# Performance work log

Measured on AMD Instinct MI355X. Metric: run time of the kernel, lower is better.

Reference implementation:

```python
import jax, jax.numpy as jnp
import numpy as np
from jax import lax

C = 128
HEADS = 8
HID = 256  # int(C * 2.0)
B, H, W = 8, 128, 128
EPS_LN = 1e-5
EPS_NORM = 1e-12


def _dwconv(x, w, pad):
    # x: [B,C,H,W], w: [C,1,kh,kw] depthwise
    return lax.conv_general_dilated(
        x, w, window_strides=(1, 1), padding=[(pad, pad), (pad, pad)],
        dimension_numbers=("NCHW", "OIHW", "NCHW"), feature_group_count=x.shape[1])


def _conv1x1(x, w):
    # w: [O, I] pointwise conv
    return jnp.einsum("oi,bihw->bohw", w, x)


def _layernorm_c(x, gamma, beta):
    # torch: reshape to [B, HW, C], LayerNorm over C, reshape back == LN over channel axis
    mu = jnp.mean(x, axis=1, keepdims=True)
    var = jnp.mean(jnp.square(x - mu), axis=1, keepdims=True)
    xn = (x - mu) * lax.rsqrt(var + EPS_LN)
    return xn * gamma[None, :, None, None] + beta[None, :, None, None]


def _l2norm(x):
    n = jnp.sqrt(jnp.sum(jnp.square(x), axis=-1, keepdims=True))
    return x / jnp.maximum(n, EPS_NORM)


def _mdta(x, qkv_w, qkv_dw, temperature, attn_proj):
    b, c, h, w = x.shape
    qkv = _dwconv(_conv1x1(x, qkv_w), qkv_dw, pad=1)  # [B,3C,H,W]
    q, k, v = jnp.split(qkv, 3, axis=1)
    hd = c // HEADS
    q = q.reshape(b, HEADS, hd, h * w)
    k = k.reshape(b, HEADS, hd, h * w)
    v = v.reshape(b, HEADS, hd, h * w)
    q, k = _l2norm(q), _l2norm(k)
    attn = jax.nn.softmax(jnp.einsum("bhdn,bhen->bhde", q, k) * temperature, axis=-1)
    out = jnp.einsum("bhde,bhen->bhdn", attn, v).reshape(b, c, h, w)
    return _conv1x1(out, attn_proj)


def _gdfn2(x, pin_w, c1_w, c3_w, c5_w, pout_w):
    x = _conv1x1(x, pin_w)  # [B,HID,H,W]
    x1 = x * c1_w[None, :, 0, 0, 0, None, None]  # depthwise 1x1 == per-channel scale
    x3 = _dwconv(x, c3_w, pad=1)
    x5 = _dwconv(x, c5_w, pad=2)
    g = jax.nn.gelu(x1, approximate=False)
    gated = jnp.concatenate([g * x3, g * x5], axis=1)  # [B,2*HID,H,W]
    return _conv1x1(gated, pout_w)


def setup_inputs() -> dict:
    key = jax.random.key(0)
    ks = jax.random.split(key, 12)
    s = 0.05
    return {
        "x": jax.random.normal(ks[0], (B, C, H, W), jnp.float32),
        "ln1_w": jnp.ones((C,), jnp.float32),
        "ln1_b": jnp.zeros((C,), jnp.float32),
        "qkv_w": jax.random.normal(ks[1], (3 * C, C), jnp.float32) * s,
        "qkv_dw": jax.random.normal(ks[2], (3 * C, 1, 3, 3), jnp.float32) * s,
        "temperature": jnp.ones((1, HEADS, 1, 1), jnp.float32),
        "attn_proj": jax.random.normal(ks[3], (C, C), jnp.float32) * s,
        "ln2_w": jnp.ones((C,), jnp.float32),
        "ln2_b": jnp.zeros((C,), jnp.float32),
        "pin_w": jax.random.normal(ks[4], (HID, C), jnp.float32) * s,
        "c1_w": jax.random.normal(ks[5], (HID, 1, 1, 1), jnp.float32) * s,
        "c3_w": jax.random.normal(ks[6], (HID, 1, 3, 3), jnp.float32) * s,
        "c5_w": jax.random.normal(ks[7], (HID, 1, 5, 5), jnp.float32) * s,
        "pout_w": jax.random.normal(ks[8], (C, 2 * HID), jnp.float32) * s,
    }


def reference(x, ln1_w, ln1_b, qkv_w, qkv_dw, temperature, attn_proj,
              ln2_w, ln2_b, pin_w, c1_w, c3_w, c5_w, pout_w):
    x = x + _mdta(_layernorm_c(x, ln1_w, ln1_b), qkv_w, qkv_dw, temperature, attn_proj)
    x = x + _gdfn2(_layernorm_c(x, ln2_w, ln2_b), pin_w, c1_w, c3_w, c5_w, pout_w)
    return x
```

## Files before the change

kernel.cpp:

```cpp
#include <hip/hip_runtime.h>
#include <type_traits>

typedef unsigned short ushort;
typedef unsigned int uint;
typedef __bf16 bf16x8 __attribute__((ext_vector_type(8)));
typedef unsigned short ushort8v __attribute__((ext_vector_type(8)));
typedef float f32x4 __attribute__((ext_vector_type(4)));

__device__ __forceinline__ float b2f(ushort u) {
    unsigned int x = ((unsigned int)u) << 16;
    float f;
    __builtin_memcpy(&f, &x, 4);
    return f;
}
__device__ __forceinline__ ushort f2bf(float f) {
    unsigned int x;
    __builtin_memcpy(&x, &f, 4);
    unsigned int r = x + 0x7fffu + ((x >> 16) & 1u);
    return (ushort)(r >> 16);
}
__device__ __forceinline__ float u2f_lo(uint u) {
    uint x = u << 16;
    float f;
    __builtin_memcpy(&f, &x, 4);
    return f;
}
__device__ __forceinline__ float u2f_hi(uint u) {
    uint x = u & 0xffff0000u;
    float f;
    __builtin_memcpy(&f, &x, 4);
    return f;
}
__device__ __forceinline__ uint packbf(float a, float b) {
    return (uint)f2bf(a) | ((uint)f2bf(b) << 16);
}

#define NPIX 16384
#define PSTRIDE 136

__device__ __forceinline__ size_t tadr(int b, int CH, int tile, int ch, int off) {
    return (((size_t)b * 256 + tile) * CH + ch) * 64 + off;
}

__device__ __forceinline__ void stage_plane(ushort* pl, const ushort* __restrict__ src,
                                            int b, int c, int CH, int tid) {
    uint* plu = (uint*)pl;
    for (int i = tid; i < 784; i += 256) {
        int idx;
        if (i < 136) idx = i;
        else if (i < 272) idx = 8840 + (i - 136);
        else {
            int j = i - 272;
            int r = (j >> 2) + 2;
            int cs = j & 3;
            idx = r * 68 + (cs == 0 ? 0 : 64 + cs);
        }
        plu[idx] = 0u;
    }
    for (int i = tid; i < 2048; i += 256) {
        int row = i >> 4, xg = (i & 15) << 3;
        int px0 = row * 128 + xg;
        uint4 v = *(const uint4*)&src[tadr(b, CH, px0 >> 6, c, px0 & 63)];
        uint* dst = (uint*)&pl[(row + 2) * PSTRIDE + xg + 2];
        dst[0] = v.x; dst[1] = v.y; dst[2] = v.z; dst[3] = v.w;
    }
    __syncthreads();
}

__device__ __forceinline__ void unpack12(const ushort* rowp, float* cc) {
    const uint* rp = (const uint*)rowp;
    uint4 u = *(const uint4*)rp;
    uint2 v = *(const uint2*)(rp + 4);
    cc[0] = u2f_lo(u.x); cc[1] = u2f_hi(u.x);
    cc[2] = u2f_lo(u.y); cc[3] = u2f_hi(u.y);
    cc[4] = u2f_lo(u.z); cc[5] = u2f_hi(u.z);
    cc[6] = u2f_lo(u.w); cc[7] = u2f_hi(u.w);
    cc[8] = u2f_lo(v.x); cc[9] = u2f_hi(v.x);
    cc[10] = u2f_lo(v.y); cc[11] = u2f_hi(v.y);
}

__global__ __launch_bounds__(256) void wcvt(const float* __restrict__ s0, ushort* __restrict__ d0, int n0,
                                            const float* __restrict__ s1, ushort* __restrict__ d1, int n1,
                                            const float* __restrict__ s2, ushort* __restrict__ d2, int n2) {
    int i = blockIdx.x * 256 + threadIdx.x;
    if (i < n0) d0[i] = f2bf(s0[i]);
    else if (i < n0 + n1) d1[i - n0] = f2bf(s1[i - n0]);
    else if (i < n0 + n1 + n2) d2[i - n0 - n1] = f2bf(s2[i - n0 - n1]);
}

template <int O, typename TIN>
__global__ __launch_bounds__(256) void ln_gemm_mfma(const TIN* __restrict__ xin,
                                                    const ushort* __restrict__ Wb,
                                                    const float* __restrict__ gamma,
                                                    const float* __restrict__ beta,
                                                    ushort* __restrict__ out) {
    __shared__ ushort xs[64][136];
    __shared__ float red[2][4][64];
    __shared__ float mu[64], rs[64];
    __shared__ float gl[128], bl[128];

    const int blk = blockIdx.x;
    const int b = blk >> 8;
    const int tile = blk & 255;
    const int tid = threadIdx.x;

    if constexpr (std::is_same<TIN, float>::value) {
        const float* xb = xin + (size_t)b * 128 * NPIX + tile * 64;
        for (int i = tid; i < 1024; i += 256) {
            int p = i & 63, cg = i >> 6;
            const float* src = xb + (size_t)(cg * 8) * NPIX + p;
            ushort8v u;
#pragma unroll
            for (int j = 0; j < 8; j++) u[j] = f2bf(src[(size_t)j * NPIX]);
            *(ushort8v*)&xs[p][cg * 8] = u;
        }
    } else {
        const ushort* xb = xin + tadr(b, 128, tile, 0, 0);
        for (int i = tid; i < 1024; i += 256) {
            int p = i & 63, cg = i >> 6;
            ushort8v u;
#pragma unroll
            for (int j = 0; j < 8; j++) u[j] = xb[(cg * 8 + j) * 64 + p];
            *(ushort8v*)&xs[p][cg * 8] = u;
        }
    }
    if (tid < 128) {
        gl[tid] = gamma[tid];
        bl[tid] = beta[tid];
    }
    __syncthreads();

    {
        const int p = tid & 63, part = tid >> 6;
        float s = 0.f, ss = 0.f;
#pragma unroll
        for (int q = 0; q < 4; q++) {
            ushort8v u = *(const ushort8v*)&xs[p][part * 32 + q * 8];
#pragma unroll
            for (int j = 0; j < 8; j++) {
                float v = b2f(u[j]);
                s += v;
                ss += v * v;
            }
        }
        red[0][part][p] = s;
        red[1][part][p] = ss;
    }
    __syncthreads();
    if (tid < 64) {
        float s = red[0][0][tid] + red[0][1][tid] + red[0][2][tid] + red[0][3][tid];
        float ss = red[1][0][tid] + red[1][1][tid] + red[1][2][tid] + red[1][3][tid];
        float m = s * (1.f / 128.f);
        float var = ss * (1.f / 128.f) - m * m;
        mu[tid] = m;
        rs[tid] = rsqrtf(var + 1e-5f);
    }
    __syncthreads();
    {
        const int p = tid & 63, part = tid >> 6;
        const float mp = mu[p], rp = rs[p];
#pragma unroll
        for (int q = 0; q < 4; q++) {
            int c0 = part * 32 + q * 8;
            ushort8v u = *(const ushort8v*)&xs[p][c0];
            ushort8v o;
#pragma unroll
            for (int j = 0; j < 8; j++) {
                float v = b2f(u[j]);
                o[j] = f2bf((v - mp) * rp * gl[c0 + j] + bl[c0 + j]);
            }
            *(ushort8v*)&xs[p][c0] = o;
        }
    }
    __syncthreads();

    const int wv = tid >> 6, lane = tid & 63;
    const int lr = lane & 15, lg = lane >> 4;

    bf16x8 bfr[4][4];
#pragma unroll
    for (int t = 0; t < 4; t++)
#pragma unroll
        for (int kc = 0; kc < 4; kc++)
            bfr[t][kc] = __builtin_bit_cast(bf16x8, *(const ushort8v*)&xs[t * 16 + lr][kc * 32 + lg * 8]);

    constexpr int MT = O / 64;
#pragma unroll 1
    for (int mt = 0; mt < MT; mt++) {
        const int o0 = (wv * MT + mt) * 16;
        bf16x8 afr[4];
#pragma unroll
        for (int kc = 0; kc < 4; kc++)
            afr[kc] = __builtin_bit_cast(bf16x8,
                *(const ushort8v*)&Wb[(size_t)(o0 + lr) * 128 + kc * 32 + lg * 8]);
        f32x4 acc[4] = {{0.f, 0.f, 0.f, 0.f}, {0.f, 0.f, 0.f, 0.f}, {0.f, 0.f, 0.f, 0.f}, {0.f, 0.f, 0.f, 0.f}};
#pragma unroll
        for (int kc = 0; kc < 4; kc++)
#pragma unroll
            for (int t = 0; t < 4; t++)
                acc[t] = __builtin_amdgcn_mfma_f32_16x16x32_bf16(afr[kc], bfr[t][kc], acc[t], 0, 0, 0);
#pragma unroll
        for (int t = 0; t < 4; t++)
#pragma unroll
            for (int r = 0; r < 4; r++) {
                int o = o0 + lg * 4 + r;
                out[tadr(b, O, tile, o, t * 16 + lr)] = f2bf(acc[t][r]);
            }
    }
}

__global__ __launch_bounds__(256) void dwconv3_lds(const ushort* __restrict__ in,
                                                   const float* __restrict__ wdw,
                                                   ushort* __restrict__ out, int CH) {
    __shared__ ushort pl[132 * PSTRIDE];
    const int c = blockIdx.x;
    const int b = blockIdx.y;
    const int tid = threadIdx.x;

    float w[9];
#pragma unroll
    for (int j = 0; j < 9; j++) w[j] = wdw[c * 9 + j];

    stage_plane(pl, in, b, c, CH, tid);

    const int x = (tid & 15) * 8;
    const int ybase = tid >> 4;
#pragma unroll 1
    for (int k = 0; k < 8; k++) {
        const int y = k * 16 + ybase;
        float a[8];
#pragma unroll
        for (int p = 0; p < 8; p++) a[p] = 0.f;
#pragma unroll
        for (int ky = 0; ky < 3; ky++) {
            float cc[12];
            unpack12(&pl[(y + ky + 1) * PSTRIDE + x], cc);
#pragma unroll
            for (int kx = 0; kx < 3; kx++) {
                float wv = w[ky * 3 + kx];
#pragma unroll
                for (int p = 0; p < 8; p++) a[p] += cc[p + kx + 1] * wv;
            }
        }
        const int px0 = (y << 7) + x;
        uint4 o;
        o.x = packbf(a[0], a[1]);
        o.y = packbf(a[2], a[3]);
        o.z = packbf(a[4], a[5]);
        o.w = packbf(a[6], a[7]);
        *(uint4*)&out[tadr(b, CH, px0 >> 6, c, px0 & 63)] = o;
    }
}

__global__ __launch_bounds__(256) void dw_gated(const ushort* __restrict__ t,
                                                const float* __restrict__ w3_,
                                                const float* __restrict__ w5_,
                                                const float* __restrict__ c1w,
                                                ushort* __restrict__ gated) {
    __shared__ ushort pl[132 * PSTRIDE];
    const int c = blockIdx.x;
    const int b = blockIdx.y;
    const int tid = threadIdx.x;

    float w3[9], w5[25];
#pragma unroll
    for (int j = 0; j < 9; j++) w3[j] = w3_[c * 9 + j];
#pragma unroll
    for (int j = 0; j < 25; j++) w5[j] = w5_[c * 25 + j];
    const float c1v = c1w[c];

    stage_plane(pl, t, b, c, 256, tid);

    const int x = (tid & 15) * 8;
    const int ybase = tid >> 4;
#pragma unroll 1
    for (int k = 0; k < 8; k++) {
        const int y = k * 16 + ybase;
        float a5[8], a3[8], tc[8];
#pragma unroll
        for (int p = 0; p < 8; p++) { a5[p] = 0.f; a3[p] = 0.f; }
#pragma unroll
        for (int ky = 0; ky < 5; ky++) {
            float cc[12];
            unpack12(&pl[(y + ky) * PSTRIDE + x], cc);
#pragma unroll
            for (int kx = 0; kx < 5; kx++) {
                float wv = w5[ky * 5 + kx];
#pragma unroll
                for (int p = 0; p < 8; p++) a5[p] += cc[p + kx] * wv;
            }
            if (ky >= 1 && ky <= 3) {
#pragma unroll
                for (int kx = 0; kx < 3; kx++) {
                    float wv = w3[(ky - 1) * 3 + kx];
#pragma unroll
                    for (int p = 0; p < 8; p++) a3[p] += cc[p + kx + 1] * wv;
                }
            }
            if (ky == 2) {
#pragma unroll
                for (int p = 0; p < 8; p++) tc[p] = cc[p + 2];
            }
        }
        const int px0 = (y << 7) + x;
        uint4 o3, o5;
        float g[8];
#pragma unroll
        for (int p = 0; p < 8; p++) {
            float x1 = tc[p] * c1v;
            g[p] = x1 * __builtin_amdgcn_rcpf(1.f + __expf(-1.702f * x1));
        }
        o3.x = packbf(g[0] * a3[0], g[1] * a3[1]);
        o3.y = packbf(g[2] * a3[2], g[3] * a3[3]);
        o3.z = packbf(g[4] * a3[4], g[5] * a3[5]);
        o3.w = packbf(g[6] * a3[6], g[7] * a3[7]);
        o5.x = packbf(g[0] * a5[0], g[1] * a5[1]);
        o5.y = packbf(g[2] * a5[2], g[3] * a5[3]);
        o5.z = packbf(g[4] * a5[4], g[5] * a5[5]);
        o5.w = packbf(g[6] * a5[6], g[7] * a5[7]);
        *(uint4*)&gated[tadr(b, 512, px0 >> 6, c, px0 & 63)] = o3;
        *(uint4*)&gated[tadr(b, 512, px0 >> 6, 256 + c, px0 & 63)] = o5;
    }
}

__global__ __launch_bounds__(256) void attn_M(const ushort* __restrict__ qkv,
                                              const float* __restrict__ temp,
                                              const float* __restrict__ attn_proj,
                                              ushort* __restrict__ M) {
    __shared__ float Sp[4][16][16];
    __shared__ float QSS[4][16], KSS[4][16];
    __shared__ float A[16][17];

    const int bh = blockIdx.x, b = bh >> 3, h = bh & 7;
    const int tid = threadIdx.x;
    const int w = tid >> 6, lane = tid & 63;
    const int lr = lane & 15, lg = lane >> 4;

    const size_t qbase = (((size_t)b * 256 + w * 64) * 384 + h * 16 + lr) * 64 + lg * 8;
    const size_t kbase = qbase + (size_t)128 * 64;

    f32x4 acc = {0.f, 0.f, 0.f, 0.f};
    f32x4 accq = {0.f, 0.f, 0.f, 0.f};
    f32x4 acck = {0.f, 0.f, 0.f, 0.f};
#pragma unroll 2
    for (int it = 0; it < 128; it++) {
        size_t off = (size_t)(it >> 1) * (384 * 64) + (it & 1) * 32;
        bf16x8 qf = __builtin_bit_cast(bf16x8, *(const ushort8v*)(qkv + qbase + off));
        bf16x8 kf = __builtin_bit_cast(bf16x8, *(const ushort8v*)(qkv + kbase + off));
        acc = __builtin_amdgcn_mfma_f32_16x16x32_bf16(qf, kf, acc, 0, 0, 0);
        accq = __builtin_amdgcn_mfma_f32_16x16x32_bf16(qf, qf, accq, 0, 0, 0);
        acck = __builtin_amdgcn_mfma_f32_16x16x32_bf16(kf, kf, acck, 0, 0, 0);
    }
#pragma unroll
    for (int r = 0; r < 4; r++) Sp[w][lg * 4 + r][lr] = acc[r];
    if (lg == (lr >> 2)) {
        QSS[w][lr] = accq[lr & 3];
        KSS[w][lr] = acck[lr & 3];
    }
    __syncthreads();

    const int d = tid >> 4, e = tid & 15;
    float S = Sp[0][d][e] + Sp[1][d][e] + Sp[2][d][e] + Sp[3][d][e];
    float nq = fmaxf(sqrtf(QSS[0][d] + QSS[1][d] + QSS[2][d] + QSS[3][d]), 1e-12f);
    float nk = fmaxf(sqrtf(KSS[0][e] + KSS[1][e] + KSS[2][e] + KSS[3][e]), 1e-12f);
    float logit = S / (nq * nk) * temp[h];
    float m = logit;
    for (int off = 8; off; off >>= 1) m = fmaxf(m, __shfl_xor(m, off, 64));
    float ex = expf(logit - m);
    float sum = ex;
    for (int off = 8; off; off >>= 1) sum += __shfl_xor(sum, off, 64);
    A[d][e] = ex / sum;
    __syncthreads();

    for (int i = tid; i < 2048; i += 256) {
        int o = i >> 4, ee = i & 15;
        float acc2 = 0.f;
#pragma unroll
        for (int dd = 0; dd < 16; dd++) acc2 += attn_proj[o * 128 + h * 16 + dd] * A[dd][ee];
        M[((size_t)b * 128 + o) * 128 + h * 16 + ee] = f2bf(acc2);
    }
}

__global__ __launch_bounds__(256) void mv_res_mfma(const ushort* __restrict__ qkv,
                                                   const ushort* __restrict__ Mb16,
                                                   const float* __restrict__ x,
                                                   ushort* __restrict__ x2) {
    __shared__ ushort vs[64][136];
    const int blk = blockIdx.x;
    const int b = blk >> 8;
    const int tile = blk & 255;
    const int tid = threadIdx.x;

    const ushort* vb = qkv + tadr(b, 384, tile, 256, 0);
    for (int i = tid; i < 1024; i += 256) {
        int p = i & 63, cg = i >> 6;
        ushort8v u;
#pragma unroll
        for (int j = 0; j < 8; j++) u[j] = vb[(cg * 8 + j) * 64 + p];
        *(ushort8v*)&vs[p][cg * 8] = u;
    }
    __syncthreads();

    const int wv = tid >> 6, lane = tid & 63;
    const int lr = lane & 15, lg = lane >> 4;

    bf16x8 bfr[4][4];
#pragma unroll
    for (int t = 0; t < 4; t++)
#pragma unroll
        for (int kc = 0; kc < 4; kc++)
            bfr[t][kc] = __builtin_bit_cast(bf16x8, *(const ushort8v*)&vs[t * 16 + lr][kc * 32 + lg * 8]);

    const ushort* Mb = Mb16 + (size_t)b * 128 * 128;
#pragma unroll 1
    for (int mt = 0; mt < 2; mt++) {
        const int o0 = (wv * 2 + mt) * 16;
        bf16x8 afr[4];
#pragma unroll
        for (int kc = 0; kc < 4; kc++)
            afr[kc] = __builtin_bit_cast(bf16x8,
                *(const ushort8v*)&Mb[(size_t)(o0 + lr) * 128 + kc * 32 + lg * 8]);
        f32x4 acc[4] = {{0.f, 0.f, 0.f, 0.f}, {0.f, 0.f, 0.f, 0.f}, {0.f, 0.f, 0.f, 0.f}, {0.f, 0.f, 0.f, 0.f}};
#pragma unroll
        for (int kc = 0; kc < 4; kc++)
#pragma unroll
            for (int t = 0; t < 4; t++)
                acc[t] = __builtin_amdgcn_mfma_f32_16x16x32_bf16(afr[kc], bfr[t][kc], acc[t], 0, 0, 0);
#pragma unroll
        for (int t = 0; t < 4; t++)
#pragma unroll
            for (int r = 0; r < 4; r++) {
                int o = o0 + lg * 4 + r;
                float xv = x[((size_t)b * 128 + o) * NPIX + tile * 64 + t * 16 + lr];
                x2[tadr(b, 128, tile, o, t * 16 + lr)] = f2bf(xv + acc[t][r]);
            }
    }
}

__global__ __launch_bounds__(256) void gdfn_mfma(const ushort* __restrict__ gated,
                                                 const ushort* __restrict__ x2,
                                                 const ushort* __restrict__ pout_b,
                                                 float* __restrict__ out) {
    __shared__ ushort gs[64][72];

    const int blk = blockIdx.x;
    const int b = blk >> 8;
    const int tile = blk & 255;
    const int tid = threadIdx.x;
    const int wv = tid >> 6, lane = tid & 63;
    const int lr = lane & 15, lg = lane >> 4;

    const ushort* gb = gated + tadr(b, 512, tile, 0, 0);

    f32x4 acc[2][4];
#pragma unroll
    for (int mt = 0; mt < 2; mt++)
#pragma unroll
        for (int tt = 0; tt < 4; tt++) acc[mt][tt] = (f32x4){0.f, 0.f, 0.f, 0.f};

#pragma unroll 1
    for (int kb = 0; kb < 8; kb++) {
        __syncthreads();
        for (int i = tid; i < 512; i += 256) {
            int p = i & 63, kg = i >> 6;
            const ushort* src = gb + (kb * 64 + kg * 8) * 64 + p;
            ushort8v u;
#pragma unroll
            for (int j = 0; j < 8; j++) u[j] = src[j * 64];
            *(ushort8v*)&gs[p][kg * 8] = u;
        }
        __syncthreads();

        bf16x8 bfrg[4][2];
#pragma unroll
        for (int tt = 0; tt < 4; tt++)
#pragma unroll
            for (int kc = 0; kc < 2; kc++)
                bfrg[tt][kc] = __builtin_bit_cast(bf16x8, *(const ushort8v*)&gs[tt * 16 + lr][kc * 32 + lg * 8]);

#pragma unroll
        for (int mt = 0; mt < 2; mt++) {
            const int o0 = (wv * 2 + mt) * 16;
            bf16x8 afr[2];
#pragma unroll
            for (int kc = 0; kc < 2; kc++)
                afr[kc] = __builtin_bit_cast(bf16x8,
                    *(const ushort8v*)&pout_b[(size_t)(o0 + lr) * 512 + kb * 64 + kc * 32 + lg * 8]);
#pragma unroll
            for (int kc = 0; kc < 2; kc++)
#pragma unroll
                for (int tt = 0; tt < 4; tt++)
                    acc[mt][tt] = __builtin_amdgcn_mfma_f32_16x16x32_bf16(afr[kc], bfrg[tt][kc], acc[mt][tt], 0, 0, 0);
        }
    }

#pragma unroll
    for (int mt = 0; mt < 2; mt++)
#pragma unroll
        for (int tt = 0; tt < 4; tt++)
#pragma unroll
            for (int r = 0; r < 4; r++) {
                int o = (wv * 2 + mt) * 16 + lg * 4 + r;
                float xv = b2f(x2[tadr(b, 128, tile, o, tt * 16 + lr)]);
                out[((size_t)b * 128 + o) * NPIX + tile * 64 + tt * 16 + lr] = xv + acc[mt][tt][r];
            }
}

extern "C" void kernel_launch(void* const* d_in, const int* in_sizes, int n_in,
                              void* d_out, int out_size, void* d_ws, size_t ws_size,
                              hipStream_t stream) {
    const float* x = (const float*)d_in[0];
    const float* ln1_w = (const float*)d_in[1];
    const float* ln1_b = (const float*)d_in[2];
    const float* qkv_w = (const float*)d_in[3];
    const float* qkv_dw = (const float*)d_in[4];
    const float* temperature = (const float*)d_in[5];
    const float* attn_proj = (const float*)d_in[6];
    const float* ln2_w = (const float*)d_in[7];
    const float* ln2_b = (const float*)d_in[8];
    const float* pin_w = (const float*)d_in[9];
    const float* c1_w = (const float*)d_in[10];
    const float* c3_w = (const float*)d_in[11];
    const float* c5_w = (const float*)d_in[12];
    const float* pout_w = (const float*)d_in[13];
    float* out = (float*)d_out;

    char* ws = (char*)d_ws;
    ushort* qkv_pre = (ushort*)(ws + 0);
    ushort* qkv     = (ushort*)(ws + 100663296);
    ushort* x2      = (ushort*)(ws + 201326592);
    ushort* t       = (ushort*)(ws + 0);
    ushort* gated   = (ushort*)(ws + 67108864);
    ushort* Mb16    = (ushort*)(ws + 235151360);
    ushort* qkv_wb  = (ushort*)(ws + 235413504);
    ushort* pin_wb  = (ushort*)(ws + 235511808);
    ushort* pout_wb = (ushort*)(ws + 235577344);

    wcvt<<<576, 256, 0, stream>>>(qkv_w, qkv_wb, 49152, pin_w, pin_wb, 32768, pout_w, pout_wb, 65536);
    ln_gemm_mfma<384, float><<<2048, 256, 0, stream>>>(x, qkv_wb, ln1_w, ln1_b, qkv_pre);
    dwconv3_lds<<<dim3(384, 8), 256, 0, stream>>>(qkv_pre, qkv_dw, qkv, 384);
    attn_M<<<64, 256, 0, stream>>>(qkv, temperature, attn_proj, Mb16);
    mv_res_mfma<<<2048, 256, 0, stream>>>(qkv, Mb16, x, x2);
    ln_gemm_mfma<256, ushort><<<2048, 256, 0, stream>>>(x2, pin_wb, ln2_w, ln2_b, t);
    dw_gated<<<dim3(256, 8), 256, 0, stream>>>(t, c3_w, c5_w, c1_w, gated);
    gdfn_mfma<<<2048, 256, 0, stream>>>(gated, x2, pout_wb, out);
}
```

Measured before the change: 324.8 us.

## Fuse attention output, residual, LayerNorm2 and pin GEMM; double-buffer gdfn staging

Merges the M·V residual kernel with the second LayerNorm and pin-projection GEMM so x2 stays in LDS instead of being written and reloaded. x2 is stored pixel-major for vectorized access in the final residual. The gated-input staging in gdfn_mfma is double-buffered with register prefetch to overlap loads with MFMA work, and V/gated loads switch to vector global reads with scattered LDS writes. This removes one launch and an x2 round trip, at the cost of more LDS per block and possible LDS bank conflicts from transposed writes.

After: 320.3 us. About the same (-1.4%).

```diff
diff --git a/kernel.cpp b/kernel.cpp
--- a/kernel.cpp
+++ b/kernel.cpp
@@ -40,6 +40,9 @@
 
 __device__ __forceinline__ size_t tadr(int b, int CH, int tile, int ch, int off) {
     return (((size_t)b * 256 + tile) * CH + ch) * 64 + off;
+}
+__device__ __forceinline__ size_t padr(int b, int tile, int p, int c) {
+    return (((size_t)b * 256 + tile) * 64 + p) * 128 + c;
 }
 
 __device__ __forceinline__ void stage_plane(ushort* pl, const ushort* __restrict__ src,
@@ -88,8 +91,8 @@
     else if (i < n0 + n1 + n2) d2[i - n0 - n1] = f2bf(s2[i - n0 - n1]);
 }
 
-template <int O, typename TIN>
-__global__ __launch_bounds__(256) void ln_gemm_mfma(const TIN* __restrict__ xin,
+template <int O>
+__global__ __launch_bounds__(256) void ln_gemm_mfma(const float* __restrict__ xin,
                                                     const ushort* __restrict__ Wb,
                                                     const float* __restrict__ gamma,
                                                     const float* __restrict__ beta,
@@ -104,25 +107,14 @@
     const int tile = blk & 255;
     const int tid = threadIdx.x;
 
-    if constexpr (std::is_same<TIN, float>::value) {
-        const float* xb = xin + (size_t)b * 128 * NPIX + tile * 64;
-        for (int i = tid; i < 1024; i += 256) {
-            int p = i & 63, cg = i >> 6;
-            const float* src = xb + (size_t)(cg * 8) * NPIX + p;
-            ushort8v u;
-#pragma unroll
-            for (int j = 0; j < 8; j++) u[j] = f2bf(src[(size_t)j * NPIX]);
-            *(ushort8v*)&xs[p][cg * 8] = u;
-        }
-    } else {
-        const ushort* xb = xin + tadr(b, 128, tile, 0, 0);
-        for (int i = tid; i < 1024; i += 256) {
-            int p = i & 63, cg = i >> 6;
-            ushort8v u;
-#pragma unroll
-            for (int j = 0; j < 8; j++) u[j] = xb[(cg * 8 + j) * 64 + p];
-            *(ushort8v*)&xs[p][cg * 8] = u;
-        }
+    const float* xb = xin + (size_t)b * 128 * NPIX + tile * 64;
+    for (int i = tid; i < 1024; i += 256) {
+        int p = i & 63, cg = i >> 6;
+        const float* src = xb + (size_t)(cg * 8) * NPIX + p;
+        ushort8v u;
+#pragma unroll
+        for (int j = 0; j < 8; j++) u[j] = f2bf(src[(size_t)j * NPIX]);
+        *(ushort8v*)&xs[p][cg * 8] = u;
     }
     if (tid < 128) {
         gl[tid] = gamma[tid];
@@ -381,67 +373,19 @@
     }
 }
 
-__global__ __launch_bounds__(256) void mv_res_mfma(const ushort* __restrict__ qkv,
-                                                   const ushort* __restrict__ Mb16,
-                                                   const float* __restrict__ x,
-                                                   ushort* __restrict__ x2) {
+__global__ __launch_bounds__(256) void mv_ln_mfma(const ushort* __restrict__ qkv,
+                                                  const ushort* __restrict__ Mb16,
+                                                  const float* __restrict__ x,
+                                                  const ushort* __restrict__ pin_b,
+                                                  const float* __restrict__ gamma,
+                                                  const float* __restrict__ beta,
+                                                  ushort* __restrict__ x2,
+                                                  ushort* __restrict__ t_out) {
     __shared__ ushort vs[64][136];
-    const int blk = blockIdx.x;
-    const int b = blk >> 8;
-    const int tile = blk & 255;
-    const int tid = threadIdx.x;
-
-    const ushort* vb = qkv + tadr(b, 384, tile, 256, 0);
-    for (int i = tid; i < 1024; i += 256) {
-        int p = i & 63, cg = i >> 6;
-        ushort8v u;
-#pragma unroll
-        for (int j = 0; j < 8; j++) u[j] = vb[(cg * 8 + j) * 64 + p];
-        *(ushort8v*)&vs[p][cg * 8] = u;
-    }
-    __syncthreads();
-
-    const int wv = tid >> 6, lane = tid & 63;
-    const int lr = lane & 15, lg = lane >> 4;
-
-    bf16x8 bfr[4][4];
-#pragma unroll
-    for (int t = 0; t < 4; t++)
-#pragma unroll
-        for (int kc = 0; kc < 4; kc++)
-            bfr[t][kc] = __builtin_bit_cast(bf16x8, *(const ushort8v*)&vs[t * 16 + lr][kc * 32 + lg * 8]);
-
-    const ushort* Mb = Mb16 + (size_t)b * 128 * 128;
-#pragma unroll 1
-    for (int mt = 0; mt < 2; mt++) {
-        const int o0 = (wv * 2 + mt) * 16;
-        bf16x8 afr[4];
-#pragma unroll
-        for (int kc = 0; kc < 4; kc++)
-            afr[kc] = __builtin_bit_cast(bf16x8,
-                *(const ushort8v*)&Mb[(size_t)(o0 + lr) * 128 + kc * 32 + lg * 8]);
-        f32x4 acc[4] = {{0.f, 0.f, 0.f, 0.f}, {0.f, 0.f, 0.f, 0.f}, {0.f, 0.f, 0.f, 0.f}, {0.f, 0.f, 0.f, 0.f}};
-#pragma unroll
-        for (int kc = 0; kc < 4; kc++)
-#pragma unroll
-            for (int t = 0; t < 4; t++)
-                acc[t] = __builtin_amdgcn_mfma_f32_16x16x32_bf16(afr[kc], bfr[t][kc], acc[t], 0, 0, 0);
-#pragma unroll
-        for (int t = 0; t < 4; t++)
-#pragma unroll
-            for (int r = 0; r < 4; r++) {
-                int o = o0 + lg * 4 + r;
-                float xv = x[((size_t)b * 128 + o) * NPIX + tile * 64 + t * 16 + lr];
-                x2[tadr(b, 128, tile, o, t * 16 + lr)] = f2bf(xv + acc[t][r]);
-            }
-    }
-}
-
-__global__ __launch_bounds__(256) void gdfn_mfma(const ushort* __restrict__ gated,
-                                                 const ushort* __restrict__ x2,
-                                                 const ushort* __restrict__ pout_b,
-                                                 float* __restrict__ out) {
-    __shared__ ushort gs[64][72];
+    __shared__ ushort xs[64][136];
+    __shared__ float red[2][4][64];
+    __shared__ float mu[64], rs[64];
+    __shared__ float gl[128], bl[128];
 
     const int blk = blockIdx.x;
     const int b = blk >> 8;
@@ -450,33 +394,184 @@
     const int wv = tid >> 6, lane = tid & 63;
     const int lr = lane & 15, lg = lane >> 4;
 
+    const ushort* vb = qkv + tadr(b, 384, tile, 256, 0);
+#pragma unroll
+    for (int k = 0; k < 4; k++) {
+        int idx = tid + k * 256;
+        int c = idx & 127, pg = idx >> 7;
+        ushort8v u = *(const ushort8v*)&vb[c * 64 + pg * 8];
+#pragma unroll
+        for (int j = 0; j < 8; j++) vs[pg * 8 + j][c] = u[j];
+    }
+    if (tid < 128) {
+        gl[tid] = gamma[tid];
+        bl[tid] = beta[tid];
+    }
+    __syncthreads();
+
+    bf16x8 bfr[4][4];
+#pragma unroll
+    for (int t = 0; t < 4; t++)
+#pragma unroll
+        for (int kc = 0; kc < 4; kc++)
+            bfr[t][kc] = __builtin_bit_cast(bf16x8, *(const ushort8v*)&vs[t * 16 + lr][kc * 32 + lg * 8]);
+
+    const ushort* Mb = Mb16 + (size_t)b * 128 * 128;
+#pragma unroll 1
+    for (int mt = 0; mt < 2; mt++) {
+        const int o0 = (wv * 2 + mt) * 16;
+        bf16x8 afr[4];
+#pragma unroll
+        for (int kc = 0; kc < 4; kc++)
+            afr[kc] = __builtin_bit_cast(bf16x8,
+                *(const ushort8v*)&Mb[(size_t)(o0 + lr) * 128 + kc * 32 + lg * 8]);
+        f32x4 acc[4] = {{0.f, 0.f, 0.f, 0.f}, {0.f, 0.f, 0.f, 0.f}, {0.f, 0.f, 0.f, 0.f}, {0.f, 0.f, 0.f, 0.f}};
+#pragma unroll
+        for (int kc = 0; kc < 4; kc++)
+#pragma unroll
+            for (int t = 0; t < 4; t++)
+                acc[t] = __builtin_amdgcn_mfma_f32_16x16x32_bf16(afr[kc], bfr[t][kc], acc[t], 0, 0, 0);
+#pragma unroll
+        for (int t = 0; t < 4; t++) {
+            int px = t * 16 + lr;
+            const float* xp = &x[((size_t)b * 128 + o0 + lg * 4) * NPIX + tile * 64 + px];
+            uint2 pk;
+            pk.x = packbf(xp[0] + acc[t][0], xp[NPIX] + acc[t][1]);
+            pk.y = packbf(xp[2 * NPIX] + acc[t][2], xp[3 * NPIX] + acc[t][3]);
+            *(uint2*)&xs[px][o0 + lg * 4] = pk;
+        }
+    }
+    __syncthreads();
+
+#pragma unroll
+    for (int k = 0; k < 4; k++) {
+        int idx = tid + k * 256;
+        int p = idx >> 4, seg = idx & 15;
+        uint4 v = *(const uint4*)&xs[p][seg * 8];
+        *(uint4*)&x2[padr(b, tile, p, seg * 8)] = v;
+    }
+    {
+        const int p = tid & 63, part = tid >> 6;
+        float s = 0.f, ss = 0.f;
+#pragma unroll
+        for (int q = 0; q < 4; q++) {
+            ushort8v u = *(const ushort8v*)&xs[p][part * 32 + q * 8];
+#pragma unroll
+            for (int j = 0; j < 8; j++) {
+                float v = b2f(u[j]);
+                s += v;
+                ss += v * v;
+            }
+        }
+        red[0][part][p] = s;
+        red[1][part][p] = ss;
+    }
+    __syncthreads();
+    if (tid < 64) {
+        float s = red[0][0][tid] + red[0][1][tid] + red[0][2][tid] + red[0][3][tid];
+        float ss = red[1][0][tid] + red[1][1][tid] + red[1][2][tid] + red[1][3][tid];
+        float m = s * (1.f / 128.f);
+        float var = ss * (1.f / 128.f) - m * m;
+        mu[tid] = m;
+        rs[tid] = rsqrtf(var + 1e-5f);
+    }
+    __syncthreads();
+    {
+        const int p = tid & 63, part = tid >> 6;
+        const float mp = mu[p], rp = rs[p];
+#pragma unroll
+        for (int q = 0; q < 4; q++) {
+            int c0 = part * 32 + q * 8;
+            ushort8v u = *(const ushort8v*)&xs[p][c0];
+            ushort8v o;
+#pragma unroll
+            for (int j = 0; j < 8; j++) {
+                float v = b2f(u[j]);
+                o[j] = f2bf((v - mp) * rp * gl[c0 + j] + bl[c0 + j]);
+            }
+            *(ushort8v*)&xs[p][c0] = o;
+        }
+    }
+    __syncthreads();
+
+    bf16x8 bfr2[4][4];
+#pragma unroll
+    for (int t = 0; t < 4; t++)
+#pragma unroll
+        for (int kc = 0; kc < 4; kc++)
+            bfr2[t][kc] = __builtin_bit_cast(bf16x8, *(const ushort8v*)&xs[t * 16 + lr][kc * 32 + lg * 8]);
+
+#pragma unroll 1
+    for (int mt = 0; mt < 4; mt++) {
+        const int o0 = (wv * 4 + mt) * 16;
+        bf16x8 afr[4];
+#pragma unroll
+        for (int kc = 0; kc < 4; kc++)
+            afr[kc] = __builtin_bit_cast(bf16x8,
+                *(const ushort8v*)&pin_b[(size_t)(o0 + lr) * 128 + kc * 32 + lg * 8]);
+        f32x4 acc[4] = {{0.f, 0.f, 0.f, 0.f}, {0.f, 0.f, 0.f, 0.f}, {0.f, 0.f, 0.f, 0.f}, {0.f, 0.f, 0.f, 0.f}};
+#pragma unroll
+        for (int kc = 0; kc < 4; kc++)
+#pragma unroll
+            for (int t = 0; t < 4; t++)
+                acc[t] = __builtin_amdgcn_mfma_f32_16x16x32_bf16(afr[kc], bfr2[t][kc], acc[t], 0, 0, 0);
+#pragma unroll
+        for (int t = 0; t < 4; t++)
+#pragma unroll
+            for (int r = 0; r < 4; r++) {
+                int o = o0 + lg * 4 + r;
+                t_out[tadr(b, 256, tile, o, t * 16 + lr)] = f2bf(acc[t][r]);
+            }
+    }
+}
+
+__global__ __launch_bounds__(256) void gdfn_mfma(const ushort* __restrict__ gated,
+                                                 const ushort* __restrict__ x2,
+                                                 const ushort* __restrict__ pout_b,
+                                                 float* __restrict__ out) {
+    __shared__ ushort gs[2][64][72];
+
+    const int blk = blockIdx.x;
+    const int b = blk >> 8;
+    const int tile = blk & 255;
+    const int tid = threadIdx.x;
+    const int wv = tid >> 6, lane = tid & 63;
+    const int lr = lane & 15, lg = lane >> 4;
+
     const ushort* gb = gated + tadr(b, 512, tile, 0, 0);
+    const int c0 = tid & 63;
+    const int pg0 = tid >> 6;
 
     f32x4 acc[2][4];
 #pragma unroll
     for (int mt = 0; mt < 2; mt++)
 #pragma unroll
         for (int tt = 0; tt < 4; tt++) acc[mt][tt] = (f32x4){0.f, 0.f, 0.f, 0.f};
+
+    ushort8v pre0 = *(const ushort8v*)&gb[c0 * 64 + pg0 * 8];
+    ushort8v pre1 = *(const ushort8v*)&gb[c0 * 64 + (pg0 + 4) * 8];
+#pragma unroll
+    for (int j = 0; j < 8; j++) {
+        gs[0][pg0 * 8 + j][c0] = pre0[j];
+        gs[0][(pg0 + 4) * 8 + j][c0] = pre1[j];
+    }
+    __syncthreads();
 
 #pragma unroll 1
     for (int kb = 0; kb < 8; kb++) {
-        __syncthreads();
-        for (int i = tid; i < 512; i += 256) {
-            int p = i & 63, kg = i >> 6;
-            const ushort* src = gb + (kb * 64 + kg * 8) * 64 + p;
-            ushort8v u;
-#pragma unroll
-            for (int j = 0; j < 8; j++) u[j] = src[j * 64];
-            *(ushort8v*)&gs[p][kg * 8] = u;
-        }
-        __syncthreads();
+        const int cur = kb & 1;
+        if (kb < 7) {
+            const ushort* nb = gb + (kb + 1) * 64 * 64;
+            pre0 = *(const ushort8v*)&nb[c0 * 64 + pg0 * 8];
+            pre1 = *(const ushort8v*)&nb[c0 * 64 + (pg0 + 4) * 8];
+        }
 
         bf16x8 bfrg[4][2];
 #pragma unroll
         for (int tt = 0; tt < 4; tt++)
 #pragma unroll
             for (int kc = 0; kc < 2; kc++)
-                bfrg[tt][kc] = __builtin_bit_cast(bf16x8, *(const ushort8v*)&gs[tt * 16 + lr][kc * 32 + lg * 8]);
+                bfrg[tt][kc] = __builtin_bit_cast(bf16x8, *(const ushort8v*)&gs[cur][tt * 16 + lr][kc * 32 + lg * 8]);
 
 #pragma unroll
         for (int mt = 0; mt < 2; mt++) {
@@ -492,18 +587,32 @@
                 for (int tt = 0; tt < 4; tt++)
                     acc[mt][tt] = __builtin_amdgcn_mfma_f32_16x16x32_bf16(afr[kc], bfrg[tt][kc], acc[mt][tt], 0, 0, 0);
         }
+
+        if (kb < 7) {
+#pragma unroll
+            for (int j = 0; j < 8; j++) {
+                gs[cur ^ 1][pg0 * 8 + j][c0] = pre0[j];
+                gs[cur ^ 1][(pg0 + 4) * 8 + j][c0] = pre1[j];
+            }
+        }
+        __syncthreads();
     }
 
 #pragma unroll
     for (int mt = 0; mt < 2; mt++)
 #pragma unroll
-        for (int tt = 0; tt < 4; tt++)
-#pragma unroll
-            for (int r = 0; r < 4; r++) {
-                int o = (wv * 2 + mt) * 16 + lg * 4 + r;
-                float xv = b2f(x2[tadr(b, 128, tile, o, tt * 16 + lr)]);
-                out[((size_t)b * 128 + o) * NPIX + tile * 64 + tt * 16 + lr] = xv + acc[mt][tt][r];
-            }
+        for (int tt = 0; tt < 4; tt++) {
+            int o0 = (wv * 2 + mt) * 16 + lg * 4;
+            int px = tt * 16 + lr;
+            uint2 xw = *(const uint2*)&x2[padr(b, tile, px, o0)];
+            float xv0 = u2f_lo(xw.x), xv1 = u2f_hi(xw.x);
+            float xv2 = u2f_lo(xw.y), xv3 = u2f_hi(xw.y);
+            size_t obase = ((size_t)b * 128 + o0) * NPIX + tile * 64 + px;
+            out[obase] = xv0 + acc[mt][tt][0];
+            out[obase + NPIX] = xv1 + acc[mt][tt][1];
+            out[obase + 2 * NPIX] = xv2 + acc[mt][tt][2];
+            out[obase + 3 * NPIX] = xv3 + acc[mt][tt][3];
+        }
 }
 
 extern "C" void kernel_launch(void* const* d_in, const int* in_sizes, int n_in,
@@ -537,11 +646,10 @@
     ushort* pout_wb = (ushort*)(ws + 235577344);
 
     wcvt<<<576, 256, 0, stream>>>(qkv_w, qkv_wb, 49152, pin_w, pin_wb, 32768, pout_w, pout_wb, 65536);
-    ln_gemm_mfma<384, float><<<2048, 256, 0, stream>>>(x, qkv_wb, ln1_w, ln1_b, qkv_pre);
+    ln_gemm_mfma<384><<<2048, 256, 0, stream>>>(x, qkv_wb, ln1_w, ln1_b, qkv_pre);
     dwconv3_lds<<<dim3(384, 8), 256, 0, stream>>>(qkv_pre, qkv_dw, qkv, 384);
     attn_M<<<64, 256, 0, stream>>>(qkv, temperature, attn_proj, Mb16);
-    mv_res_mfma<<<2048, 256, 0, stream>>>(qkv, Mb16, x, x2);
-    ln_gemm_mfma<256, ushort><<<2048, 256, 0, stream>>>(x2, pin_wb, ln2_w, ln2_b, t);
+    mv_ln_mfma<<<2048, 256, 0, stream>>>(qkv, Mb16, x, pin_wb, ln2_w, ln2_b, x2, t);
     dw_gated<<<dim3(256, 8), 256, 0, stream>>>(t, c3_w, c5_w, c1_w, gated);
     gdfn_mfma<<<2048, 256, 0, stream>>>(gated, x2, pout_wb, out);
 }
```
